# Kernel tuning notes

Measured on AMD Instinct MI355X. Metric: run time of the kernel, lower is better.

Reference implementation:

```python
import jax, jax.numpy as jnp
import numpy as np
from jax import lax

B, DIM, HEADS, H, W = 8, 64, 8, 256, 256
N_FFT = 128  # n in fft(); h//n == 2


def conv1x1(x, w):
    # x: [b,ci,h,w], w: [co,ci]
    return jnp.einsum('bchw,oc->bohw', x, w)


def conv2d(x, w, pad):
    # dense conv, w: [co,ci,kh,kw]
    return lax.conv_general_dilated(x, w, (1, 1), [(pad, pad), (pad, pad)],
                                    dimension_numbers=('NCHW', 'OIHW', 'NCHW'))


def dwconv3x3(x, w):
    # depthwise, w: [C,3,3]
    C = x.shape[1]
    return lax.conv_general_dilated(x, w[:, None], (1, 1), [(1, 1), (1, 1)],
                                    dimension_numbers=('NCHW', 'OIHW', 'NCHW'),
                                    feature_group_count=C)


def l2norm(t, eps=1e-12):
    n = jnp.sqrt(jnp.sum(t * t, axis=-1, keepdims=True))
    return t / jnp.maximum(n, eps)


def chanel_cross_attention(x, y, temp, qw, qdw, kvw, kvdw, projw):
    b, c, h, w = x.shape
    q = dwconv3x3(conv1x1(x, qw), qdw)          # [b,c,h,w]
    kv = dwconv3x3(conv1x1(y, kvw), kvdw)       # [b,2c,h,w]
    k, v = kv[:, :c], kv[:, c:]
    def rh(t):
        return t.reshape(b, HEADS, c // HEADS, h * w)
    q, k, v = rh(q), rh(k), rh(v)
    q = l2norm(q)
    k = l2norm(k)
    attn = jnp.einsum('bhcn,bhdn->bhcd', q, k) * temp  # temp [HEADS,1,1]
    attn = jax.nn.softmax(attn, axis=-1)
    out = jnp.einsum('bhcd,bhdn->bhcn', attn, v).reshape(b, c, h, w)
    return conv1x1(out, projw)


def fre_module_fft(x, conv1_w, rate_w1, rate_w2):
    x = conv2d(x, conv1_w, 1)                   # [B,DIM,H,W]
    h, w = x.shape[-2:]
    # dynamic threshold -> per-sample rectangular low-pass mask
    pooled = jnp.mean(x, axis=(2, 3))           # [B,DIM]
    t = jax.nn.gelu(pooled @ rate_w1.T, approximate=False) @ rate_w2.T
    thr = jax.nn.sigmoid(t)                     # [B,2]
    h_ = ((h // N_FFT) * thr[:, 0]).astype(jnp.int32)  # [B], trunc like .int()
    w_ = ((w // N_FFT) * thr[:, 1]).astype(jnp.int32)
    rows = jnp.arange(h)
    cols = jnp.arange(w)
    row_in = (rows[None, :] >= (h // 2 - h_)[:, None]) & (rows[None, :] < (h // 2 + h_)[:, None])
    col_in = (cols[None, :] >= (w // 2 - w_)[:, None]) & (cols[None, :] < (w // 2 + w_)[:, None])
    mask = (row_in[:, None, :, None] & col_in[:, None, None, :]).astype(x.dtype)  # [B,1,h,w]

    fft = jnp.fft.fft2(x, axes=(-2, -1), norm='forward')
    fft = jnp.roll(fft, (h // 2, w // 2), axis=(2, 3))        # shift
    def back(f):
        f = jnp.roll(f, (-(h // 2), -(w // 2)), axis=(2, 3))  # unshift
        return jnp.abs(jnp.fft.ifft2(f, axes=(-2, -1), norm='forward'))
    high = back(fft * (1.0 - mask))
    low = back(fft * mask)
    return high, low


def fre_refine(low, high, spatial_w, cg_w1, cg_w2, projw, projb):
    # SpatialGate(high)
    mx = jnp.max(high, axis=1, keepdims=True)
    mn = jnp.mean(high, axis=1, keepdims=True)
    sw = jax.nn.sigmoid(conv2d(jnp.concatenate([mx, mn], axis=1), spatial_w, 3))  # [b,1,h,w]
    # ChannelGate(low)
    def mlp(p):  # p: [b,dim]
        return (jax.nn.relu(p @ cg_w1.T) @ cg_w2.T)
    avg = mlp(jnp.mean(low, axis=(2, 3)))
    mxc = mlp(jnp.max(low, axis=(2, 3)))
    cw = jax.nn.sigmoid(avg + mxc)[:, :, None, None]  # [b,dim,1,1]
    out = low * sw + high * cw
    return conv1x1(out, projw) + projb[None, :, None, None]


def reference(x, y, conv1_w, rate_w1, rate_w2, cca_temp, cca_qw, cca_qdw,
              cca_kvw, cca_kvdw, cca_projw, spatial_w, cg_w1, cg_w2,
              refine_projw, refine_projb, para1, para2):
    b = y.shape[0]
    x = jax.image.resize(x, (b, x.shape[1], H, W), method='bilinear')
    high, low = fre_module_fft(x, conv1_w, rate_w1, rate_w2)
    def cca(i, a, bb):
        return chanel_cross_attention(a, bb, cca_temp[i], cca_qw[i], cca_qdw[i],
                                      cca_kvw[i], cca_kvdw[i], cca_projw[i])
    high = cca(0, high, y)   # channel_cross_l
    low = cca(1, low, y)     # channel_cross_h
    agg = fre_refine(low, high, spatial_w, cg_w1, cg_w2, refine_projw, refine_projb)
    out = cca(2, y, agg)     # channel_cross_agg
    return out * para1[None] + y * para2[None]


def setup_inputs() -> dict:
    key = jax.random.key(0)
    ks = jax.random.split(key, 18)
    def rn(k, shape, s=0.05):
        return jax.random.normal(k, shape, jnp.float32) * s
    return {
        'x': jax.random.normal(ks[0], (B, 3, 128, 128), jnp.float32),
        'y': jax.random.normal(ks[1], (B, DIM, H, W), jnp.float32),
        'conv1_w': rn(ks[2], (DIM, 3, 3, 3)),
        'rate_w1': rn(ks[3], (DIM // 8, DIM)),
        'rate_w2': rn(ks[4], (2, DIM // 8)),
        'cca_temp': jnp.ones((3, HEADS, 1, 1), jnp.float32),
        'cca_qw': rn(ks[5], (3, DIM, DIM)),
        'cca_qdw': rn(ks[6], (3, DIM, 3, 3)),
        'cca_kvw': rn(ks[7], (3, 2 * DIM, DIM)),
        'cca_kvdw': rn(ks[8], (3, 2 * DIM, 3, 3)),
        'cca_projw': rn(ks[9], (3, DIM, DIM)),
        'spatial_w': rn(ks[10], (1, 2, 7, 7)),
        'cg_w1': rn(ks[11], (DIM // 16, DIM)),
        'cg_w2': rn(ks[12], (DIM, DIM // 16)),
        'refine_projw': rn(ks[13], (DIM, DIM)),
        'refine_projb': rn(ks[14], (DIM,)),
        'para1': rn(ks[15], (DIM, 1, 1), 0.1),
        'para2': jnp.ones((DIM, 1, 1), jnp.float32),
    }
```

## Files before the change

kernel.cpp:

```cpp
#include <hip/hip_runtime.h>
#include <math.h>

#define HW_ 65536
#define NCHUNK 16
typedef long long i64;
#define TWO_PI 6.283185307179586476925f

typedef __bf16 bf16x8 __attribute__((ext_vector_type(8)));
typedef __bf16 bf16x4 __attribute__((ext_vector_type(4)));
typedef float f32x4 __attribute__((ext_vector_type(4)));

#define MFMA16(A,B,C) __builtin_amdgcn_mfma_f32_16x16x32_bf16(A,B,C,0,0,0)

__device__ __forceinline__ float sigm(float x){ return 1.0f/(1.0f+expf(-x)); }

__device__ __forceinline__ bf16x8 cvt_w8(const float* wp){
  float4 w0 = *(const float4*)wp;
  float4 w1 = *(const float4*)(wp+4);
  bf16x8 r;
  r[0]=(__bf16)w0.x; r[1]=(__bf16)w0.y; r[2]=(__bf16)w0.z; r[3]=(__bf16)w0.w;
  r[4]=(__bf16)w1.x; r[5]=(__bf16)w1.y; r[6]=(__bf16)w1.z; r[7]=(__bf16)w1.w;
  return r;
}

__device__ __forceinline__ void st_bf4(__bf16* p, float a, float b, float c, float d){
  bf16x4 v; v[0]=(__bf16)a; v[1]=(__bf16)b; v[2]=(__bf16)c; v[3]=(__bf16)d;
  *(bf16x4*)p = v;
}

__global__ __launch_bounds__(256) void k_resize(const float* __restrict__ x, float* __restrict__ R, int b0){
  int idx = blockIdx.x*256 + threadIdx.x;
  int ox = idx & 255;
  int oy = (idx >> 8) & 255;
  int bc = idx >> 16;
  int lb = bc/3; int c = bc - lb*3;
  float sx = ox*0.5f - 0.25f;
  float sy = oy*0.5f - 0.25f;
  int x0 = (int)floorf(sx); float fx = sx - (float)x0;
  int y0 = (int)floorf(sy); float fy = sy - (float)y0;
  int x1 = min(x0+1,127); int y1 = min(y0+1,127);
  x0 = max(x0,0); y0 = max(y0,0);
  const float* p = x + ((i64)(b0+lb)*3 + c)*16384;
  float v00=p[y0*128+x0], v01=p[y0*128+x1], v10=p[y1*128+x0], v11=p[y1*128+x1];
  R[idx] = (1.0f-fy)*((1.0f-fx)*v00 + fx*v01) + fy*((1.0f-fx)*v10 + fx*v11);
}

__global__ __launch_bounds__(256) void k_conv3(const float* __restrict__ R, const float* __restrict__ w, float* __restrict__ out){
  int y = blockIdx.x & 255; int b = blockIdx.x >> 8; int t = threadIdx.x;
  float win[27];
  #pragma unroll
  for (int ci=0;ci<3;ci++){
    #pragma unroll
    for (int ky=0;ky<3;ky++){
      int yy = y+ky-1;
      const float* ip = R + (((i64)(b*3+ci))<<16) + yy*256;
      #pragma unroll
      for (int kx=0;kx<3;kx++){
        int xx = t+kx-1;
        float v = 0.f;
        if ((unsigned)yy<256u && (unsigned)xx<256u) v = ip[xx];
        win[ci*9+ky*3+kx] = v;
      }
    }
  }
  i64 obase = ((i64)b<<22) + (y<<8) + t;
  for (int o=0;o<64;o++){
    const float* wp = w + o*27;
    float acc=0.f;
    #pragma unroll
    for (int j=0;j<27;j++) acc += wp[j]*win[j];
    out[obase + ((i64)o<<16)] = acc;
  }
}

__global__ __launch_bounds__(256) void k_dft(const float* __restrict__ xc, float* __restrict__ coeff, float* __restrict__ pooled){
  __shared__ float tc[256], ts[256];
  __shared__ float red[256];
  int t = threadIdx.x;
  float ang = TWO_PI * ((float)t/256.0f);
  tc[t] = cosf(ang); ts[t] = sinf(ang);
  __syncthreads();
  int bc = blockIdx.x;
  const float* p = xc + (i64)bc*HW_;
  float s=0, cr=0, ci=0, rr=0, ri=0, dr=0, di=0;
  for (int i=t; i<HW_; i+=256){
    float v = p[i];
    int col = i & 255, row = i >> 8, ds = (row+col)&255;
    s  += v;
    cr += v*tc[col]; ci += v*ts[col];
    rr += v*tc[row]; ri += v*ts[row];
    dr += v*tc[ds];  di += v*ts[ds];
  }
  float vals[7] = {s,cr,ci,rr,ri,dr,di};
  for (int j=0;j<7;j++){
    red[t] = vals[j]; __syncthreads();
    for (int st=128; st>0; st>>=1){ if (t<st) red[t]+=red[t+st]; __syncthreads(); }
    if (t==0) vals[j] = red[0];
    __syncthreads();
  }
  if (t==0){
    const float sc = 1.0f/65536.0f;
    for (int j=0;j<7;j++) coeff[bc*8+j] = vals[j]*sc;
    pooled[bc] = vals[0]*sc;
  }
}

__global__ __launch_bounds__(64) void k_thr(const float* __restrict__ pooled, const float* __restrict__ w1,
                      const float* __restrict__ w2, float* __restrict__ flag){
  __shared__ float hid[8];
  int b = blockIdx.x; int t = threadIdx.x;
  if (t < 8){
    float a = 0.f;
    for (int c=0;c<64;c++) a += pooled[b*64+c]*w1[t*64+c];
    hid[t] = 0.5f*a*(1.0f+erff(a*0.70710678118654752440f));
  }
  __syncthreads();
  if (t==0){
    float t0=0,t1=0;
    for (int k=0;k<8;k++){ t0 += hid[k]*w2[k]; t1 += hid[k]*w2[8+k]; }
    int h_ = (int)(2.0f*sigm(t0));
    int w_ = (int)(2.0f*sigm(t1));
    flag[b] = (h_>0 && w_>0) ? 1.0f : 0.0f;
  }
}

#define MM_COMPUTE2(Wbase, BF) \
  bf16x8 af[4][2]; \
  _Pragma("unroll") \
  for (int m=0;m<4;m++){ \
    _Pragma("unroll") \
    for (int s=0;s<2;s++) af[m][s] = cvt_w8((Wbase) + (m*16 + lm)*64 + s*32 + kg*8); \
  } \
  f32x4 acc[4][4]; \
  _Pragma("unroll") \
  for (int m=0;m<4;m++){ \
    _Pragma("unroll") \
    for (int e=0;e<4;e++){ f32x4 z = {0.f,0.f,0.f,0.f}; acc[m][e]=z; } \
  } \
  _Pragma("unroll") \
  for (int m=0;m<4;m++){ \
    _Pragma("unroll") \
    for (int e=0;e<4;e++){ \
      _Pragma("unroll") \
      for (int s=0;s<2;s++) acc[m][e] = MFMA16(af[m][s], BF[s][e], acc[m][e]); \
    } \
  }

#define MM_STORE_BF(outp) \
  _Pragma("unroll") \
  for (int m=0;m<4;m++){ \
    _Pragma("unroll") \
    for (int r=0;r<4;r++){ \
      int oc = m*16 + kg*4 + r; \
      st_bf4((outp) + ibase + ((i64)oc<<16) + 4*lm, acc[m][0][r], acc[m][1][r], acc[m][2][r], acc[m][3][r]); \
    } \
  }

#define MM_SETUP \
  int t = threadIdx.x; \
  int lane = t & 63, wvi = t >> 6; \
  i64 px0 = (i64)blockIdx.x*256 + wvi*64; \
  int b = (int)(px0 >> 16); \
  int p0 = (int)(px0 & (HW_-1)); \
  i64 ibase = ((i64)b<<22) + p0; \
  int lm = lane & 15, kg = lane >> 4;

#define X8_SETUP \
  int t = threadIdx.x; \
  int lane = t & 63, wvi = t >> 6; \
  i64 px0 = (i64)blockIdx.x*512 + (i64)wvi*128; \
  int b = (int)(px0 >> 16); \
  int p0 = (int)(px0 & (HW_-1)); \
  i64 ibase = ((i64)b<<22) + p0; \
  int lm = lane & 15, kg = lane >> 4;

#define X8_FILL_F32(in_ptr) \
  _Pragma("unroll") \
  for (int s=0;s<2;s++){ \
    _Pragma("unroll") \
    for (int j=0;j<8;j++){ \
      const float* p_ = (in_ptr) + ((i64)(s*32 + kg*8 + j)<<16) + 8*lm; \
      float4 a_ = *(const float4*)p_; \
      float4 c_ = *(const float4*)(p_+4); \
      bf[s][0][j]=(__bf16)a_.x; bf[s][1][j]=(__bf16)a_.y; bf[s][2][j]=(__bf16)a_.z; bf[s][3][j]=(__bf16)a_.w; \
      bf[s][4][j]=(__bf16)c_.x; bf[s][5][j]=(__bf16)c_.y; bf[s][6][j]=(__bf16)c_.z; bf[s][7][j]=(__bf16)c_.w; \
    } \
  }

#define X8_FILL_BF(in_ptr) \
  _Pragma("unroll") \
  for (int s=0;s<2;s++){ \
    _Pragma("unroll") \
    for (int j=0;j<8;j++){ \
      bf16x8 u_ = *(const bf16x8*)((in_ptr) + ((i64)(s*32 + kg*8 + j)<<16) + 8*lm); \
      _Pragma("unroll") \
      for (int e=0;e<8;e++) bf[s][e][j] = u_[e]; \
    } \
  }

#define X8_ACC_M(Wbase, BF) \
  bf16x8 af0 = cvt_w8((Wbase) + (m*16 + lm)*64 + kg*8); \
  bf16x8 af1 = cvt_w8((Wbase) + (m*16 + lm)*64 + 32 + kg*8); \
  f32x4 acc[8]; \
  _Pragma("unroll") \
  for (int e=0;e<8;e++){ f32x4 z_ = {0.f,0.f,0.f,0.f}; acc[e]=z_; } \
  _Pragma("unroll") \
  for (int e=0;e<8;e++){ acc[e]=MFMA16(af0,BF[0][e],acc[e]); acc[e]=MFMA16(af1,BF[1][e],acc[e]); }

#define X8_ST_BF(outp) \
  _Pragma("unroll") \
  for (int r=0;r<4;r++){ \
    int oc = m*16 + kg*4 + r; \
    bf16x8 ov; \
    _Pragma("unroll") \
    for (int e=0;e<8;e++) ov[e]=(__bf16)acc[e][r]; \
    *(bf16x8*)((outp) + ibase + ((i64)oc<<16) + 8*lm) = ov; \
  }

#define X8_MM_BF(Wbase, BF, outp) \
  _Pragma("unroll") \
  for (int m=0;m<4;m++){ X8_ACC_M(Wbase, BF) X8_ST_BF(outp) }

__global__ __launch_bounds__(256) void k_convq2(const float* __restrict__ xc, const float* __restrict__ coeff,
      const float* __restrict__ flag, const float* __restrict__ qwh, const float* __restrict__ qwl,
      __bf16* __restrict__ outh, __bf16* __restrict__ outl){
  __shared__ float tc[256], ts[256];
  {
    int tt = threadIdx.x;
    float ang = TWO_PI * ((float)tt/256.0f);
    tc[tt]=cosf(ang); ts[tt]=sinf(ang);
  }
  __syncthreads();
  MM_SETUP
  float fl = flag[b];
  int y = p0 >> 8;
  int xb = (p0 & 255) + 4*lm;
  float crow = tc[y], srow = ts[y];
  float cx[4], sx[4], cd[4], sd[4];
  #pragma unroll
  for (int e=0;e<4;e++){
    int xx = xb + e;
    cx[e]=tc[xx]; sx[e]=ts[xx];
    int d = (xx + y) & 255;
    cd[e]=tc[d]; sd[e]=ts[d];
  }
  bf16x8 bfh[2][4], bfl[2][4];
  #pragma unroll
  for (int s=0;s<2;s++){
    #pragma unroll
    for (int j=0;j<8;j++){
      int ch = s*32 + kg*8 + j;
      const float* cf = coeff + ((b<<6)+ch)*8;
      float4 ca = *(const float4*)cf;
      float4 cb = *(const float4*)(cf+4);
      float F00=ca.x, cR=ca.y, cI=ca.z, rR=ca.w, rI=cb.x, dR=cb.y, dI=cb.z;
      float4 xr = *(const float4*)(xc + ibase + ((i64)ch<<16) + 4*lm);
      float rowR = F00 + rR*crow + rI*srow;
      float rowI = rI*crow - rR*srow;
      #pragma unroll
      for (int e=0;e<4;e++){
        float re = rowR + cR*cx[e] + cI*sx[e] + dR*cd[e] + dI*sd[e];
        float im = rowI + cI*cx[e] - cR*sx[e] + dI*cd[e] - dR*sd[e];
        re*=fl; im*=fl;
        float vl = sqrtf(re*re+im*im);
        float hr = ((const float*)&xr)[e] - re;
        float vh = sqrtf(hr*hr + im*im);
        bfh[s][e][j] = (__bf16)vh;
        bfl[s][e][j] = (__bf16)vl;
      }
    }
  }
  {
    MM_COMPUTE2(qwh, bfh)
    MM_STORE_BF(outh)
  }
  {
    MM_COMPUTE2(qwl, bfl)
    MM_STORE_BF(outl)
  }
}

__global__ __launch_bounds__(256) void k_kvq(const float* __restrict__ yin,
      const float* __restrict__ kvw0, const float* __restrict__ kvw1, const float* __restrict__ qw2,
      __bf16* __restrict__ k0o, __bf16* __restrict__ v0o,
      __bf16* __restrict__ k1o, __bf16* __restrict__ v1o, __bf16* __restrict__ q2o){
  X8_SETUP
  bf16x8 bf[2][8];
  X8_FILL_F32(yin + ibase)
  X8_MM_BF(kvw0,        bf, k0o)
  X8_MM_BF(kvw0 + 4096, bf, v0o)
  X8_MM_BF(kvw1,        bf, k1o)
  X8_MM_BF(kvw1 + 4096, bf, v1o)
  X8_MM_BF(qw2,         bf, q2o)
}

__global__ __launch_bounds__(256) void k_mm_kvb(const __bf16* __restrict__ in, const float* __restrict__ w,
      __bf16* __restrict__ kout, __bf16* __restrict__ vout){
  X8_SETUP
  bf16x8 bf[2][8];
  X8_FILL_BF(in + ibase)
  X8_MM_BF(w,        bf, kout)
  X8_MM_BF(w + 4096, bf, vout)
}

__global__ __launch_bounds__(256) void k_mm_hi(const __bf16* __restrict__ v, const float* __restrict__ M,
        float* __restrict__ mx, float* __restrict__ mn, __bf16* __restrict__ out){
  X8_SETUP
  bf16x8 bf[2][8];
  X8_FILL_BF(v + ibase)
  const float* Wb = M + ((i64)b<<12);
  float smx[8], ssum[8];
  #pragma unroll
  for (int e=0;e<8;e++){ smx[e]=-1e30f; ssum[e]=0.f; }
  #pragma unroll
  for (int m=0;m<4;m++){
    X8_ACC_M(Wb, bf)
    X8_ST_BF(out)
    #pragma unroll
    for (int r=0;r<4;r++){
      #pragma unroll
      for (int e=0;e<8;e++){ smx[e]=fmaxf(smx[e],acc[e][r]); ssum[e]+=acc[e][r]; }
    }
  }
  #pragma unroll
  for (int e=0;e<8;e++){
    smx[e] = fmaxf(smx[e], __shfl_xor(smx[e],16));
    smx[e] = fmaxf(smx[e], __shfl_xor(smx[e],32));
    ssum[e] += __shfl_xor(ssum[e],16);
    ssum[e] += __shfl_xor(ssum[e],32);
  }
  if (kg==0){
    i64 pbase = ((i64)b<<16) + p0 + 8*lm;
    *(float4*)(mx+pbase)   = make_float4(smx[0],smx[1],smx[2],smx[3]);
    *(float4*)(mx+pbase+4) = make_float4(smx[4],smx[5],smx[6],smx[7]);
    const float iv = 1.0f/64.0f;
    *(float4*)(mn+pbase)   = make_float4(ssum[0]*iv,ssum[1]*iv,ssum[2]*iv,ssum[3]*iv);
    *(float4*)(mn+pbase+4) = make_float4(ssum[4]*iv,ssum[5]*iv,ssum[6]*iv,ssum[7]*iv);
  }
}

__global__ __launch_bounds__(256) void k_mm_lo(const __bf16* __restrict__ v, const float* __restrict__ M,
        __bf16* __restrict__ out, float* __restrict__ spart){
  __shared__ float ls[4][64], lmx[4][64];
  X8_SETUP
  bf16x8 bf[2][8];
  X8_FILL_BF(v + ibase)
  const float* Wb = M + ((i64)b<<12);
  #pragma unroll
  for (int m=0;m<4;m++){
    X8_ACC_M(Wb, bf)
    X8_ST_BF(out)
    #pragma unroll
    for (int r=0;r<4;r++){
      int oc = m*16 + kg*4 + r;
      float s = 0.f, mm = -1e30f;
      #pragma unroll
      for (int e=0;e<8;e++){ s += acc[e][r]; mm = fmaxf(mm, acc[e][r]); }
      #pragma unroll
      for (int off=8; off; off>>=1){ s += __shfl_xor(s,off); mm = fmaxf(mm,__shfl_xor(mm,off)); }
      if (lm==0){ ls[wvi][oc]=s; lmx[wvi][oc]=mm; }
    }
  }
  __syncthreads();
  if (t<64){
    float s = ls[0][t]+ls[1][t]+ls[2][t]+ls[3][t];
    float mm = fmaxf(fmaxf(lmx[0][t],lmx[1][t]),fmaxf(lmx[2][t],lmx[3][t]));
    spart[(i64)blockIdx.x*128 + t*2]   = s;
    spart[(i64)blockIdx.x*128 + t*2+1] = mm;
  }
}

__global__ __launch_bounds__(256) void k_mm_comb(const __bf16* __restrict__ lo2, const __bf16* __restrict__ hi2,
        const float* __restrict__ swb, const float* __restrict__ cwv,
        const float* __restrict__ w, const float* __restrict__ bias, __bf16* __restrict__ out){
  X8_SETUP
  const float* swp = swb + ((i64)b<<16) + p0 + 8*lm;
  float4 sw0 = *(const float4*)swp;
  float4 sw1 = *(const float4*)(swp+4);
  float swv[8] = {sw0.x,sw0.y,sw0.z,sw0.w,sw1.x,sw1.y,sw1.z,sw1.w};
  bf16x8 bf[2][8];
  #pragma unroll
  for (int s=0;s<2;s++){
    #pragma unroll
    for (int j=0;j<8;j++){
      int ch = s*32 + kg*8 + j;
      bf16x8 l8 = *(const bf16x8*)(lo2 + ibase + ((i64)ch<<16) + 8*lm);
      bf16x8 h8 = *(const bf16x8*)(hi2 + ibase + ((i64)ch<<16) + 8*lm);
      float cw = cwv[(b<<6) + ch];
      #pragma unroll
      for (int e=0;e<8;e++) bf[s][e][j] = (__bf16)((float)l8[e]*swv[e] + (float)h8[e]*cw);
    }
  }
  #pragma unroll
  for (int m=0;m<4;m++){
    X8_ACC_M(w, bf)
    #pragma unroll
    for (int r=0;r<4;r++){
      int oc = m*16 + kg*4 + r;
      float bv = bias[oc];
      bf16x8 ov;
      #pragma unroll
      for (int e=0;e<8;e++) ov[e]=(__bf16)(acc[e][r]+bv);
      *(bf16x8*)(out + ibase + ((i64)oc<<16) + 8*lm) = ov;
    }
  }
}

__global__ __launch_bounds__(256) void k_mm_fin(const __bf16* __restrict__ v, const float* __restrict__ M,
      const float* __restrict__ para1, const float* __restrict__ para2,
      const float* __restrict__ yin, float* __restrict__ out){
  X8_SETUP
  bf16x8 bf[2][8];
  X8_FILL_BF(v + ibase)
  const float* Wb = M + ((i64)b<<12);
  #pragma unroll
  for (int m=0;m<4;m++){
    X8_ACC_M(Wb, bf)
    #pragma unroll
    for (int r=0;r<4;r++){
      int oc = m*16 + kg*4 + r;
      float p1 = para1[oc], p2 = para2[oc];
      const float* yp = yin + ibase + ((i64)oc<<16) + 8*lm;
      float4 y0 = *(const float4*)yp;
      float4 y1 = *(const float4*)(yp+4);
      float* op = out + ibase + ((i64)oc<<16) + 8*lm;
      *(float4*)op     = make_float4(acc[0][r]*p1+y0.x*p2, acc[1][r]*p1+y0.y*p2,
                                     acc[2][r]*p1+y0.z*p2, acc[3][r]*p1+y0.w*p2);
      *(float4*)(op+4) = make_float4(acc[4][r]*p1+y1.x*p2, acc[5][r]*p1+y1.y*p2,
                                     acc[6][r]*p1+y1.z*p2, acc[7][r]*p1+y1.w*p2);
    }
  }
}

__global__ __launch_bounds__(256) void k_gram(const __bf16* __restrict__ q0, const __bf16* __restrict__ kk0,
        const __bf16* __restrict__ q1, const __bf16* __restrict__ kk1,
        const float* __restrict__ qdw0, const float* __restrict__ kdw0,
        const float* __restrict__ qdw1, const float* __restrict__ kdw1,
        float* __restrict__ part, int hgrid){
  __shared__ float red[4][16][16];
  int bx = blockIdx.x;
  int set = (bx >= hgrid) ? 1 : 0;
  int blk = bx - set*hgrid;
  const __bf16* qpre = set ? q1 : q0;
  const __bf16* kpre = set ? kk1 : kk0;
  const float* qdw = set ? qdw1 : qdw0;
  const float* kdw = set ? kdw1 : kdw0;
  float* ppart = part + (i64)set*hgrid*80;
  int rowblk = blk & 15;
  int bh = blk >> 4;
  int h = bh & 7, b = bh >> 3;
  int t = threadIdx.x;
  int lane = t & 63, wvi = t >> 6;
  int lm = lane & 15, kg = lane >> 4;
  int a = lm & 7;
  const __bf16* plane = (lm < 8 ? qpre : kpre) + (((i64)((b<<6)+(h<<3)+a))<<16);
  const float* wp = (lm < 8 ? qdw : kdw) + h*72 + a*9;
  float w0=wp[0],w1=wp[1],w2=wp[2],w3=wp[3],w4=wp[4],w5=wp[5],w6=wp[6],w7=wp[7],w8=wp[8];
  int R0 = rowblk*16;
  f32x4 acc = {0.f,0.f,0.f,0.f};
  #pragma unroll
  for (int cc=0; cc<2; cc++){
    int chunk = wvi*2 + cc;
    int xb = chunk*32 + kg*8;
    bool left = (xb==0), right = (xb==248);
    float h0[8], h1[8];
    #pragma unroll
    for (int e=0;e<8;e++){ h0[e]=0.f; h1[e]=0.f; }
    for (int ir = R0-1; ir <= R0+16; ir++){
      bool rok = ((unsigned)ir < 256u);
      float win[10];
      if (rok){
        const __bf16* rp = plane + ir*256 + xb;
        bf16x8 mid = *(const bf16x8*)rp;
        win[0] = left ? 0.f : (float)rp[-1];
        #pragma unroll
        for (int w=1; w<9; w++) win[w] = (float)mid[w-1];
        win[9] = right ? 0.f : (float)rp[8];
      } else {
        #pragma unroll
        for (int w=0; w<10; w++) win[w] = 0.f;
      }
      float o[8];
      #pragma unroll
      for (int e=0;e<8;e++){
        float t0 = w0*win[e] + w1*win[e+1] + w2*win[e+2];
        float t1 = w3*win[e] + w4*win[e+1] + w5*win[e+2];
        float t2 = w6*win[e] + w7*win[e+1] + w8*win[e+2];
        o[e] = h0[e] + t2;
        h0[e] = h1[e] + t1;
        h1[e] = t0;
      }
      if (ir > R0){
        bf16x8 xf;
        #pragma unroll
        for (int e=0;e<8;e++) xf[e] = (__bf16)o[e];
        acc = MFMA16(xf, xf, acc);
      }
    }
  }
  #pragma unroll
  for (int r=0;r<4;r++) red[wvi][kg*4+r][lm] = acc[r];
  __syncthreads();
  if (t < 80){
    int r, c;
    if (t < 64){ r = t>>3; c = 8 + (t&7); }
    else if (t < 72){ r = t-64; c = r; }
    else { r = 8 + (t-72); c = r; }
    float s = red[0][r][c]+red[1][r][c]+red[2][r][c]+red[3][r][c];
    ppart[(i64)blk*80 + t] = s;
  }
}

__global__ __launch_bounds__(128) void k_stats_fin(const float* __restrict__ part, float* __restrict__ stats){
  int bh = blockIdx.x; int t = threadIdx.x;
  if (t < 80){
    float s=0.f;
    for (int c=0;c<NCHUNK;c++) s += part[((i64)bh*NCHUNK+c)*80 + t];
    stats[bh*80+t] = s;
  }
}

__global__ __launch_bounds__(64) void k_attn_m(const float* __restrict__ stats, const float* __restrict__ temp,
                         const float* __restrict__ projw, float* __restrict__ M, int nb){
  __shared__ float attn[8][8][8];
  int bsup = blockIdx.x; int t = threadIdx.x;
  int set = (bsup >= nb) ? 1 : 0;
  int h = t >> 3, cc = t & 7;
  const float* st = stats + (bsup*8+h)*80;
  float nq = fmaxf(sqrtf(st[64+cc]), 1e-12f);
  float tmp = temp[set*8 + h];
  const float* pw = projw + set*4096;
  float s[8];
  float mx = -1e30f;
  #pragma unroll
  for (int d=0;d<8;d++){
    float nk = fmaxf(sqrtf(st[72+d]), 1e-12f);
    s[d] = st[cc*8+d]/(nq*nk)*tmp;
    mx = fmaxf(mx, s[d]);
  }
  float sum=0.f;
  #pragma unroll
  for (int d=0;d<8;d++){ s[d]=expf(s[d]-mx); sum+=s[d]; }
  float inv = 1.0f/sum;
  #pragma unroll
  for (int d=0;d<8;d++) attn[h][cc][d] = s[d]*inv;
  __syncthreads();
  int o = t;
  for (int hh=0; hh<8; hh++){
    #pragma unroll
    for (int d=0; d<8; d++){
      float acc=0.f;
      #pragma unroll
      for (int c2=0;c2<8;c2++) acc += pw[o*64 + hh*8 + c2]*attn[hh][c2][d];
      M[((i64)bsup*64 + o)*64 + hh*8 + d] = acc;
    }
  }
}

__global__ __launch_bounds__(256) void k_dwb(const __bf16* __restrict__ in0, const __bf16* __restrict__ in1,
        const float* __restrict__ wd0, const float* __restrict__ wd1,
        __bf16* __restrict__ out0, __bf16* __restrict__ out1, int hgrid){
  int bx = blockIdx.x;
  int set = (bx >= hgrid) ? 1 : 0;
  int blk = bx - set*hgrid;
  const __bf16* in = set ? in1 : in0;
  const float* wd = set ? wd1 : wd0;
  __bf16* out = set ? out1 : out0;
  int half = blk & 1; int c = (blk>>1)&63; int b = blk>>7;
  int t = threadIdx.x;
  int strip = t & 31, rg = t >> 5;
  const __bf16* ip = in + (((i64)((b<<6)+c))<<16);
  __bf16* op = out + (((i64)((b<<6)+c))<<16);
  const float* wp = wd + c*9;
  float w0=wp[0],w1=wp[1],w2=wp[2],w3=wp[3],w4=wp[4],w5=wp[5],w6=wp[6],w7=wp[7],w8=wp[8];
  int R0 = half*128 + rg*16;
  int xb = strip*8;
  bool left = (xb==0), right = (xb==248);
  float h0[8], h1[8];
  #pragma unroll
  for (int e=0;e<8;e++){ h0[e]=0.f; h1[e]=0.f; }
  for (int ir = R0-1; ir <= R0+16; ir++){
    bool rok = ((unsigned)ir < 256u);
    float win[10];
    if (rok){
      const __bf16* rp = ip + ir*256 + xb;
      bf16x8 mid = *(const bf16x8*)rp;
      win[0] = left ? 0.f : (float)rp[-1];
      #pragma unroll
      for (int w=1; w<9; w++) win[w] = (float)mid[w-1];
      win[9] = right ? 0.f : (float)rp[8];
    } else {
      #pragma unroll
      for (int w=0; w<10; w++) win[w] = 0.f;
    }
    float o[8];
    #pragma unroll
    for (int e=0;e<8;e++){
      float t0 = w0*win[e] + w1*win[e+1] + w2*win[e+2];
      float t1 = w3*win[e] + w4*win[e+1] + w5*win[e+2];
      float t2 = w6*win[e] + w7*win[e+1] + w8*win[e+2];
      o[e] = h0[e] + t2;
      h0[e] = h1[e] + t1;
      h1[e] = t0;
    }
    if (ir > R0){
      bf16x8 ov;
      #pragma unroll
      for (int e=0;e<8;e++) ov[e] = (__bf16)o[e];
      *(bf16x8*)(op + (ir-1)*256 + xb) = ov;
    }
  }
}

__global__ __launch_bounds__(64) void k_spatfin(const float* __restrict__ spart, float* __restrict__ lmean, float* __restrict__ lmax){
  int b = blockIdx.x; int c = threadIdx.x;
  float s=0.f, m=-1e30f;
  for (int r=0;r<128;r++){
    s += spart[(i64)(b*128+r)*128 + c*2];
    m = fmaxf(m, spart[(i64)(b*128+r)*128 + c*2+1]);
  }
  lmean[b*64+c] = s*(1.0f/65536.0f);
  lmax[b*64+c]  = m;
}

__global__ __launch_bounds__(64) void k_cw(const float* __restrict__ mean, const float* __restrict__ mxv,
                     const float* __restrict__ w1, const float* __restrict__ w2, float* __restrict__ cw){
  __shared__ float ha[4], hm[4];
  int b = blockIdx.x; int t = threadIdx.x;
  if (t < 4){
    float sa=0.f, sm_=0.f;
    for (int c=0;c<64;c++){ sa += w1[t*64+c]*mean[b*64+c]; sm_ += w1[t*64+c]*mxv[b*64+c]; }
    ha[t] = fmaxf(sa, 0.f); hm[t] = fmaxf(sm_, 0.f);
  }
  __syncthreads();
  float a=0.f;
  #pragma unroll
  for (int j=0;j<4;j++) a += w2[t*4+j]*(ha[j]+hm[j]);
  cw[b*64+t] = sigm(a);
}

__global__ __launch_bounds__(256) void k_sw(const float* __restrict__ mx, const float* __restrict__ mn,
                     const float* __restrict__ w, float* __restrict__ sw){
  int row = blockIdx.x & 255; int b = blockIdx.x >> 8; int t = threadIdx.x;
  const float* m0 = mx + ((i64)b<<16);
  const float* m1 = mn + ((i64)b<<16);
  float acc=0.f;
  for (int ky=0;ky<7;ky++){
    int yy = row+ky-3; if ((unsigned)yy>255u) continue;
    for (int kx=0;kx<7;kx++){
      int xx = t+kx-3; if ((unsigned)xx>255u) continue;
      acc += w[ky*7+kx]*m0[yy*256+xx] + w[49+ky*7+kx]*m1[yy*256+xx];
    }
  }
  sw[((i64)b<<16) + row*256 + t] = sigm(acc);
}

extern "C" void kernel_launch(void* const* d_in, const int* in_sizes, int n_in,
                              void* d_out, int out_size, void* d_ws, size_t ws_size,
                              hipStream_t stream){
  const float* x      = (const float*)d_in[0];
  const float* y      = (const float*)d_in[1];
  const float* conv1w = (const float*)d_in[2];
  const float* ratew1 = (const float*)d_in[3];
  const float* ratew2 = (const float*)d_in[4];
  const float* temp   = (const float*)d_in[5];
  const float* qw     = (const float*)d_in[6];
  const float* qdw    = (const float*)d_in[7];
  const float* kvw    = (const float*)d_in[8];
  const float* kvdw   = (const float*)d_in[9];
  const float* projw  = (const float*)d_in[10];
  const float* spw    = (const float*)d_in[11];
  const float* cgw1   = (const float*)d_in[12];
  const float* cgw2   = (const float*)d_in[13];
  const float* rprojw = (const float*)d_in[14];
  const float* rprojb = (const float*)d_in[15];
  const float* para1  = (const float*)d_in[16];
  const float* para2  = (const float*)d_in[17];
  float* D = (float*)d_out;

  int nb = 8;
  for (;;){
    size_t unit = (size_t)nb*64*HW_;
    size_t pool = (size_t)nb*3*HW_
                + (size_t)nb*512 + (size_t)nb*64 + 64
                + 2*(size_t)nb*8*NCHUNK*80
                + 2*(size_t)nb*8*80
                + 2*(size_t)nb*64*64
                + 3*(size_t)nb*HW_
                + (size_t)nb*128*128
                + 3*(size_t)nb*64;
    if ((3*unit + pool)*sizeof(float) <= ws_size || nb==1) break;
    nb >>= 1;
  }

  size_t unit = (size_t)nb*64*HW_;
  float* U0 = (float*)d_ws;
  float* U1 = U0 + unit;
  float* U2 = U1 + unit;
  float* sm = U2 + unit;
  float* Rbuf  = sm;  sm += (size_t)nb*3*HW_;
  float* coeff = sm;  sm += (size_t)nb*512;
  float* pooled= sm;  sm += (size_t)nb*64;
  float* flagb = sm;  sm += 64;
  float* part  = sm;  sm += 2*(size_t)nb*8*NCHUNK*80;
  float* stats = sm;  sm += 2*(size_t)nb*8*80;
  float* Mb    = sm;  sm += 2*(size_t)nb*64*64;
  float* mxmap = sm;  sm += (size_t)nb*HW_;
  float* mnmap = sm;  sm += (size_t)nb*HW_;
  float* swb   = sm;  sm += (size_t)nb*HW_;
  float* spart = sm;  sm += (size_t)nb*128*128;
  float* lmean = sm;  sm += (size_t)nb*64;
  float* lmax  = sm;  sm += (size_t)nb*64;
  float* cwb   = sm;  sm += (size_t)nb*64;

  int hgr = nb*8*NCHUNK;
  int hdw = nb*128;

  for (int b0 = 0; b0 < 8; b0 += nb){
    const float* yg = y + (i64)b0*64*HW_;
    float*       Dg = D + (i64)b0*64*HW_;
    __bf16* U0a = (__bf16*)U0; __bf16* U0c = U0a + unit;
    __bf16* U1a = (__bf16*)U1; __bf16* U1c = U1a + unit;
    __bf16* U2a = (__bf16*)U2; __bf16* U2c = U2a + unit;
    __bf16* Dga = (__bf16*)Dg; __bf16* Dgc = Dga + unit;
    float* Mb1 = Mb + (i64)nb*4096;

    k_resize <<<nb*3*256, 256,0,stream>>>(x, Rbuf, b0);
    k_conv3  <<<nb*256,   256,0,stream>>>(Rbuf, conv1w, U0);
    k_dft    <<<nb*64,    256,0,stream>>>(U0, coeff, pooled);
    k_thr    <<<nb,       64, 0,stream>>>(pooled, ratew1, ratew2, flagb);

    k_convq2 <<<nb*256,256,0,stream>>>(U0, coeff, flagb, qw + 0*4096, qw + 1*4096, U1a, U1c);
    k_kvq    <<<nb*128,256,0,stream>>>(yg, kvw + 0*8192, kvw + 1*8192, qw + 2*4096,
                                       U2a, Dga, U2c, Dgc, U0c);

    k_gram   <<<2*hgr,256,0,stream>>>(U1a, U2a, U1c, U2c,
                                      qdw + 0*576, kvdw + 0*1152, qdw + 1*576, kvdw + 1*1152,
                                      part, hgr);
    k_stats_fin<<<2*nb*8, 128,0,stream>>>(part, stats);
    k_dwb    <<<2*hdw,256,0,stream>>>(Dga, Dgc, kvdw + 0*1152 + 576, kvdw + 1*1152 + 576,
                                      U1a, U1c, hdw);
    k_attn_m <<<2*nb, 64,0,stream>>>(stats, temp, projw, Mb, nb);

    k_mm_hi  <<<nb*128,256,0,stream>>>(U1a, Mb,  mxmap, mnmap, Dga);
    k_mm_lo  <<<nb*128,256,0,stream>>>(U1c, Mb1, Dgc, spart);

    k_spatfin <<<nb,     64, 0,stream>>>(spart, lmean, lmax);
    k_cw      <<<nb,     64, 0,stream>>>(lmean, lmax, cgw1, cgw2, cwb);
    k_sw      <<<nb*256, 256,0,stream>>>(mxmap, mnmap, spw, swb);
    k_mm_comb<<<nb*128,256,0,stream>>>(Dgc, Dga, swb, cwb, rprojw, rprojb, U0a);

    k_mm_kvb <<<nb*128,256,0,stream>>>(U0a, kvw + 2*8192, U2a, U2c);
    k_gram   <<<hgr,256,0,stream>>>(U0c, U2a, U0c, U2a,
                                    qdw + 2*576, kvdw + 2*1152, qdw + 2*576, kvdw + 2*1152,
                                    part, hgr);
    k_stats_fin<<<nb*8, 128,0,stream>>>(part, stats);
    k_dwb    <<<hdw,256,0,stream>>>(U2c, U2c, kvdw + 2*1152 + 576, kvdw + 2*1152 + 576,
                                    U1a, U1a, hdw);
    k_attn_m <<<nb, 64,0,stream>>>(stats, temp + 2*8, projw + 2*4096, Mb, nb);
    k_mm_fin <<<nb*128,256,0,stream>>>(U1a, Mb, para1, para2, yg, Dg);
  }
}
```

Baseline: 889.7 us.

## Store conv3 output as bf16 and stage gram rows through double-buffered LDS

The 3x3 conv output feeding the DFT and convq2 kernels is now stored as bf16 instead of fp32, halving that intermediate's write and read traffic. The Gram kernel now cooperatively loads each input row of 16 planes into a double-buffered LDS tile and prefetches the next row while computing the current one, instead of each lane doing unaligned global loads with halo reads. This adds a block barrier per row and reduces the precision of the conv output, which feeds the high-frequency residual computed in convq2.

Result: faster. 774.3 us (-13.0%).

```diff
diff --git a/kernel.cpp b/kernel.cpp
--- a/kernel.cpp
+++ b/kernel.cpp
@@ -45,7 +45,7 @@
   R[idx] = (1.0f-fy)*((1.0f-fx)*v00 + fx*v01) + fy*((1.0f-fx)*v10 + fx*v11);
 }
 
-__global__ __launch_bounds__(256) void k_conv3(const float* __restrict__ R, const float* __restrict__ w, float* __restrict__ out){
+__global__ __launch_bounds__(256) void k_conv3(const float* __restrict__ R, const float* __restrict__ w, __bf16* __restrict__ out){
   int y = blockIdx.x & 255; int b = blockIdx.x >> 8; int t = threadIdx.x;
   float win[27];
   #pragma unroll
@@ -69,11 +69,11 @@
     float acc=0.f;
     #pragma unroll
     for (int j=0;j<27;j++) acc += wp[j]*win[j];
-    out[obase + ((i64)o<<16)] = acc;
-  }
-}
-
-__global__ __launch_bounds__(256) void k_dft(const float* __restrict__ xc, float* __restrict__ coeff, float* __restrict__ pooled){
+    out[obase + ((i64)o<<16)] = (__bf16)acc;
+  }
+}
+
+__global__ __launch_bounds__(256) void k_dft(const __bf16* __restrict__ xc, float* __restrict__ coeff, float* __restrict__ pooled){
   __shared__ float tc[256], ts[256];
   __shared__ float red[256];
   int t = threadIdx.x;
@@ -81,10 +81,10 @@
   tc[t] = cosf(ang); ts[t] = sinf(ang);
   __syncthreads();
   int bc = blockIdx.x;
-  const float* p = xc + (i64)bc*HW_;
+  const __bf16* p = xc + (i64)bc*HW_;
   float s=0, cr=0, ci=0, rr=0, ri=0, dr=0, di=0;
   for (int i=t; i<HW_; i+=256){
-    float v = p[i];
+    float v = (float)p[i];
     int col = i & 255, row = i >> 8, ds = (row+col)&255;
     s  += v;
     cr += v*tc[col]; ci += v*ts[col];
@@ -221,7 +221,7 @@
   _Pragma("unroll") \
   for (int m=0;m<4;m++){ X8_ACC_M(Wbase, BF) X8_ST_BF(outp) }
 
-__global__ __launch_bounds__(256) void k_convq2(const float* __restrict__ xc, const float* __restrict__ coeff,
+__global__ __launch_bounds__(256) void k_convq2(const __bf16* __restrict__ xc, const float* __restrict__ coeff,
       const float* __restrict__ flag, const float* __restrict__ qwh, const float* __restrict__ qwl,
       __bf16* __restrict__ outh, __bf16* __restrict__ outl){
   __shared__ float tc[256], ts[256];
@@ -254,7 +254,7 @@
       float4 ca = *(const float4*)cf;
       float4 cb = *(const float4*)(cf+4);
       float F00=ca.x, cR=ca.y, cI=ca.z, rR=ca.w, rI=cb.x, dR=cb.y, dI=cb.z;
-      float4 xr = *(const float4*)(xc + ibase + ((i64)ch<<16) + 4*lm);
+      bf16x4 xr4 = *(const bf16x4*)(xc + ibase + ((i64)ch<<16) + 4*lm);
       float rowR = F00 + rR*crow + rI*srow;
       float rowI = rI*crow - rR*srow;
       #pragma unroll
@@ -263,7 +263,7 @@
         float im = rowI + cI*cx[e] - cR*sx[e] + dI*cd[e] - dR*sd[e];
         re*=fl; im*=fl;
         float vl = sqrtf(re*re+im*im);
-        float hr = ((const float*)&xr)[e] - re;
+        float hr = (float)xr4[e] - re;
         float vh = sqrtf(hr*hr + im*im);
         bfh[s][e][j] = (__bf16)vh;
         bfl[s][e][j] = (__bf16)vl;
@@ -437,6 +437,7 @@
         const float* __restrict__ qdw0, const float* __restrict__ kdw0,
         const float* __restrict__ qdw1, const float* __restrict__ kdw1,
         float* __restrict__ part, int hgrid){
+  __shared__ __bf16 lds[2][16][264];
   __shared__ float red[4][16][16];
   int bx = blockIdx.x;
   int set = (bx >= hgrid) ? 1 : 0;
@@ -452,43 +453,56 @@
   int t = threadIdx.x;
   int lane = t & 63, wvi = t >> 6;
   int lm = lane & 15, kg = lane >> 4;
-  int a = lm & 7;
-  const __bf16* plane = (lm < 8 ? qpre : kpre) + (((i64)((b<<6)+(h<<3)+a))<<16);
-  const float* wp = (lm < 8 ? qdw : kdw) + h*72 + a*9;
+  const float* wp = (lm < 8 ? qdw : kdw) + h*72 + (lm&7)*9;
   float w0=wp[0],w1=wp[1],w2=wp[2],w3=wp[3],w4=wp[4],w5=wp[5],w6=wp[6],w7=wp[7],w8=wp[8];
+  int p = t >> 4, seg = t & 15;
+  const __bf16* plbase = (p < 8 ? qpre : kpre) + (((i64)((b<<6)+(h<<3)+(p&7)))<<16);
   int R0 = rowblk*16;
+
+  float h0c[2][8], h1c[2][8];
+  #pragma unroll
+  for (int cc=0;cc<2;cc++)
+    #pragma unroll
+    for (int e=0;e<8;e++){ h0c[cc][e]=0.f; h1c[cc][e]=0.f; }
   f32x4 acc = {0.f,0.f,0.f,0.f};
-  #pragma unroll
-  for (int cc=0; cc<2; cc++){
-    int chunk = wvi*2 + cc;
-    int xb = chunk*32 + kg*8;
-    bool left = (xb==0), right = (xb==248);
-    float h0[8], h1[8];
-    #pragma unroll
-    for (int e=0;e<8;e++){ h0[e]=0.f; h1[e]=0.f; }
-    for (int ir = R0-1; ir <= R0+16; ir++){
-      bool rok = ((unsigned)ir < 256u);
+
+  auto stage = [&](int bi, int ir){
+    __bf16* dst = &lds[bi][p][seg*16];
+    if ((unsigned)ir < 256u){
+      const __bf16* src = plbase + ir*256 + seg*16;
+      bf16x8 a = *(const bf16x8*)src;
+      bf16x8 c = *(const bf16x8*)(src+8);
+      *(bf16x8*)dst = a; *(bf16x8*)(dst+8) = c;
+    } else {
+      bf16x8 z = {};
+      *(bf16x8*)dst = z; *(bf16x8*)(dst+8) = z;
+    }
+  };
+
+  stage(0, R0-1);
+  __syncthreads();
+  int buf = 0;
+  for (int ir = R0-1; ir <= R0+16; ir++){
+    if (ir < R0+16) stage(buf^1, ir+1);
+    const __bf16* rowp = &lds[buf][lm][0];
+    #pragma unroll
+    for (int cc=0; cc<2; cc++){
+      int xb = (wvi*2 + cc)*32 + kg*8;
+      bf16x8 mid = *(const bf16x8*)(rowp + xb);
       float win[10];
-      if (rok){
-        const __bf16* rp = plane + ir*256 + xb;
-        bf16x8 mid = *(const bf16x8*)rp;
-        win[0] = left ? 0.f : (float)rp[-1];
-        #pragma unroll
-        for (int w=1; w<9; w++) win[w] = (float)mid[w-1];
-        win[9] = right ? 0.f : (float)rp[8];
-      } else {
-        #pragma unroll
-        for (int w=0; w<10; w++) win[w] = 0.f;
-      }
+      win[0] = (xb==0)   ? 0.f : (float)rowp[xb-1];
+      #pragma unroll
+      for (int w=1; w<9; w++) win[w] = (float)mid[w-1];
+      win[9] = (xb==248) ? 0.f : (float)rowp[xb+8];
       float o[8];
       #pragma unroll
       for (int e=0;e<8;e++){
         float t0 = w0*win[e] + w1*win[e+1] + w2*win[e+2];
         float t1 = w3*win[e] + w4*win[e+1] + w5*win[e+2];
         float t2 = w6*win[e] + w7*win[e+1] + w8*win[e+2];
-        o[e] = h0[e] + t2;
-        h0[e] = h1[e] + t1;
-        h1[e] = t0;
+        o[e] = h0c[cc][e] + t2;
+        h0c[cc][e] = h1c[cc][e] + t1;
+        h1c[cc][e] = t0;
       }
       if (ir > R0){
         bf16x8 xf;
@@ -497,6 +511,8 @@
         acc = MFMA16(xf, xf, acc);
       }
     }
+    __syncthreads();
+    buf ^= 1;
   }
   #pragma unroll
   for (int r=0;r<4;r++) red[wvi][kg*4+r][lm] = acc[r];
@@ -726,11 +742,11 @@
     float* Mb1 = Mb + (i64)nb*4096;
 
     k_resize <<<nb*3*256, 256,0,stream>>>(x, Rbuf, b0);
-    k_conv3  <<<nb*256,   256,0,stream>>>(Rbuf, conv1w, U0);
-    k_dft    <<<nb*64,    256,0,stream>>>(U0, coeff, pooled);
+    k_conv3  <<<nb*256,   256,0,stream>>>(Rbuf, conv1w, U0a);
+    k_dft    <<<nb*64,    256,0,stream>>>(U0a, coeff, pooled);
     k_thr    <<<nb,       64, 0,stream>>>(pooled, ratew1, ratew2, flagb);
 
-    k_convq2 <<<nb*256,256,0,stream>>>(U0, coeff, flagb, qw + 0*4096, qw + 1*4096, U1a, U1c);
+    k_convq2 <<<nb*256,256,0,stream>>>(U0a, coeff, flagb, qw + 0*4096, qw + 1*4096, U1a, U1c);
     k_kvq    <<<nb*128,256,0,stream>>>(yg, kvw + 0*8192, kvw + 1*8192, qw + 2*4096,
                                        U2a, Dga, U2c, Dgc, U0c);
 
```
